# Kernel tuning notes

Measured on AMD Instinct MI355X. Metric: run time of the kernel, lower is better.

The kernel has to match this reference:

```python
import jax, jax.numpy as jnp
import numpy as np

D = 64          # node/edge feature dim
DIN = 3 * D     # concat [src, edge, dst]
N_NODES = 30000
N_EDGES = 480000


def _lin_init(key, fan_in, fan_out):
    return jax.random.normal(key, (fan_in, fan_out), dtype=jnp.float32) / np.sqrt(fan_in)


def setup_inputs() -> dict:
    key = jax.random.key(0)
    ks = jax.random.split(key, 24)
    inp = {
        "node_feat": jax.random.normal(ks[0], (N_NODES, D), dtype=jnp.float32),
        "edge_feat": jax.random.normal(ks[1], (N_EDGES, D), dtype=jnp.float32),
        "src": jax.random.randint(ks[2], (N_EDGES,), 0, N_NODES, dtype=jnp.int32),
        "dst": jax.random.randint(ks[3], (N_EDGES,), 0, N_NODES, dtype=jnp.int32),
    }
    # GatedMLP params for edge update and node update: each has a 'layers' MLP
    # [192->64->64] (SiLU after both layers) and a 'gates' MLP [192->64->64]
    # (SiLU after hidden only, then sigmoid).
    i = 4
    for pref in ("edge", "node"):
        for branch in ("layers", "gates"):
            inp[f"{pref}_{branch}_W0"] = _lin_init(ks[i], DIN, D); i += 1
            inp[f"{pref}_{branch}_b0"] = jnp.zeros((D,), jnp.float32)
            inp[f"{pref}_{branch}_W1"] = _lin_init(ks[i], D, D); i += 1
            inp[f"{pref}_{branch}_b1"] = jnp.zeros((D,), jnp.float32)
    inp["node_out_W"] = _lin_init(ks[i], D, D)  # Linear(64,64,bias=False)
    return inp


def _gated_mlp(x, lW0, lb0, lW1, lb1, gW0, gb0, gW1, gb1):
    silu = jax.nn.silu
    # layers branch: activate hidden + last
    h = silu(silu(x @ lW0 + lb0) @ lW1 + lb1)
    # gates branch: activate hidden only, sigmoid at the end
    g = silu(x @ gW0 + gb0) @ gW1 + gb1
    return h * jax.nn.sigmoid(g)


def reference(node_feat, edge_feat, src, dst,
              edge_layers_W0, edge_layers_b0, edge_layers_W1, edge_layers_b1,
              edge_gates_W0, edge_gates_b0, edge_gates_W1, edge_gates_b1,
              node_layers_W0, node_layers_b0, node_layers_W1, node_layers_b1,
              node_gates_W0, node_gates_b0, node_gates_W1, node_gates_b1,
              node_out_W):
    h_src = node_feat[src]            # [E, D] gather
    h_dst = node_feat[dst]            # [E, D] gather
    # edge update: gated MLP on [src || edge || dst], residual
    e_in = jnp.concatenate([h_src, edge_feat, h_dst], axis=-1)  # [E, 3D]
    e_new = edge_feat + _gated_mlp(e_in, edge_layers_W0, edge_layers_b0,
                                   edge_layers_W1, edge_layers_b1,
                                   edge_gates_W0, edge_gates_b0,
                                   edge_gates_W1, edge_gates_b1)
    # node messages: gated MLP on [src || new_edge || dst]
    m_in = jnp.concatenate([h_src, e_new, h_dst], axis=-1)      # [E, 3D]
    msg = _gated_mlp(m_in, node_layers_W0, node_layers_b0,
                     node_layers_W1, node_layers_b1,
                     node_gates_W0, node_gates_b0,
                     node_gates_W1, node_gates_b1)
    # scatter-sum to destination nodes, output linear, residual
    agg = jax.ops.segment_sum(msg, dst, num_segments=node_feat.shape[0])
    h_new = node_feat + agg @ node_out_W
    return h_new, e_new
```

## Files before the change

### kernel.cpp

```cpp
#include <hip/hip_runtime.h>
#include <hip/hip_bf16.h>
#include <math.h>

typedef __bf16 bf16_t;
typedef __bf16 bf16x8 __attribute__((ext_vector_type(8)));
typedef float  f32x4  __attribute__((ext_vector_type(4)));

#define MFMA16(a,b,c) __builtin_amdgcn_mfma_f32_16x16x32_bf16((a),(b),(c),0,0,0)

namespace {
constexpr int D    = 64;
constexpr int DIN  = 192;
constexpr int NN   = 30000;
constexpr int NE   = 480000;

constexpr int NBLK   = 256;
constexpr int NTHR   = 512;
constexpr int NUNITS = NE / 32;
constexpr int NWAVES = NBLK * (NTHR / 64);

constexpr int W0R    = 192;
constexpr int W0T_SZ = 64 * W0R;
constexpr int SW1    = 72;
constexpr int W1T_SZ = 64 * SW1;
constexpr int HBS    = 32 * 64;

constexpr int LDS_SCR = 4 * W0T_SZ;
constexpr int LDS_TOT = LDS_SCR + 8 * HBS;

constexpr size_t WS_AGG_BYTES = (size_t)NN * D * 4;
constexpr size_t WS_WT_BYTES  = (size_t)(4 * W0T_SZ + 4 * W1T_SZ) * 2;
constexpr size_t WS_FLAG_OFF  = WS_AGG_BYTES + WS_WT_BYTES;
}

__device__ __forceinline__ bf16x8 ldA(const bf16_t* p) {
  return *(const bf16x8*)p;
}
__device__ __forceinline__ bf16x8 ldA(const float* p) {
  const float4* q4 = (const float4*)p;
  const float4 u = q4[0], v = q4[1];
  bf16x8 r;
  r[0] = (bf16_t)u.x; r[1] = (bf16_t)u.y; r[2] = (bf16_t)u.z; r[3] = (bf16_t)u.w;
  r[4] = (bf16_t)v.x; r[5] = (bf16_t)v.y; r[6] = (bf16_t)v.z; r[7] = (bf16_t)v.w;
  return r;
}

__device__ __forceinline__ float silu_f(float v) { return v / (1.f + __expf(-v)); }
__device__ __forceinline__ float sigm_f(float v) { return 1.f / (1.f + __expf(-v)); }

__device__ __forceinline__ void wfence() {
  __builtin_amdgcn_sched_barrier(0);
  asm volatile("s_waitcnt lgkmcnt(0)" ::: "memory");
  __builtin_amdgcn_sched_barrier(0);
}

__device__ __forceinline__ void mlp_l0m(f32x4 accL[2][4], f32x4 accG[2][4],
    const bf16_t* __restrict__ w0L, const bf16_t* __restrict__ w0G,
    const bf16x8 fa[6][2], const int ksw[6], int m)
{
  const f32x4 z = {0.f, 0.f, 0.f, 0.f};
  #pragma unroll
  for (int h = 0; h < 2; ++h)
    #pragma unroll
    for (int nt = 0; nt < 4; ++nt) { accL[h][nt] = z; accG[h][nt] = z; }
  __builtin_amdgcn_s_setprio(1);
  #pragma unroll
  for (int kt = 0; kt < 6; ++kt) {
    const bf16_t* pL = w0L + m * W0R + ksw[kt];
    const bf16_t* pG = w0G + m * W0R + ksw[kt];
    #pragma unroll
    for (int nt = 0; nt < 4; ++nt) {
      const bf16x8 bL = *(const bf16x8*)(pL + nt * 16 * W0R);
      const bf16x8 bG = *(const bf16x8*)(pG + nt * 16 * W0R);
      accL[0][nt] = MFMA16(fa[kt][0], bL, accL[0][nt]);
      accL[1][nt] = MFMA16(fa[kt][1], bL, accL[1][nt]);
      accG[0][nt] = MFMA16(fa[kt][0], bG, accG[0][nt]);
      accG[1][nt] = MFMA16(fa[kt][1], bG, accG[1][nt]);
    }
  }
  __builtin_amdgcn_s_setprio(0);
}

__device__ __forceinline__ void loadW1(bf16x8 wb[2][4],
                                       const bf16_t* __restrict__ w1, int m, int q) {
  #pragma unroll
  for (int kt = 0; kt < 2; ++kt)
    #pragma unroll
    for (int nt = 0; nt < 4; ++nt)
      wb[kt][nt] = ldA(w1 + (nt * 16 + m) * SW1 + kt * 32 + q * 8);
}

__device__ __forceinline__ void mlp_l1r(f32x4 acc[2][4],
    const bf16_t* __restrict__ hb, const bf16x8 wb[2][4], const int ksw[6], int m)
{
  const f32x4 z = {0.f, 0.f, 0.f, 0.f};
  #pragma unroll
  for (int h = 0; h < 2; ++h)
    #pragma unroll
    for (int nt = 0; nt < 4; ++nt) acc[h][nt] = z;
  __builtin_amdgcn_s_setprio(1);
  #pragma unroll
  for (int kt = 0; kt < 2; ++kt) {
    const bf16x8 a0 = *(const bf16x8*)(hb + m * 64 + ksw[kt]);
    const bf16x8 a1 = *(const bf16x8*)(hb + (m + 16) * 64 + ksw[kt]);
    #pragma unroll
    for (int nt = 0; nt < 4; ++nt) {
      acc[0][nt] = MFMA16(a0, wb[kt][nt], acc[0][nt]);
      acc[1][nt] = MFMA16(a1, wb[kt][nt], acc[1][nt]);
    }
  }
  __builtin_amdgcn_s_setprio(0);
}

template<typename TB>
__device__ __forceinline__ void hidden_silu(const f32x4 acc[2][4],
    const TB* __restrict__ bias, bf16_t* __restrict__ hb, int m, int q)
{
  #pragma unroll
  for (int nt = 0; nt < 4; ++nt) {
    const float bv = (float)bias[nt * 16 + m];
    #pragma unroll
    for (int h = 0; h < 2; ++h) {
      #pragma unroll
      for (int r = 0; r < 4; ++r) {
        const float v = acc[h][nt][r] + bv;
        const int row = h * 16 + q * 4 + r;
        const int col = (nt * 16 + m) ^ (((q * 4 + r) & 7) << 3);
        hb[row * 64 + col] = (bf16_t)silu_f(v);
      }
    }
  }
}

__global__ void detect_kernel(const void* w0, int* flag) {
  __shared__ int cnt;
  if (threadIdx.x == 0) cnt = 0;
  __syncthreads();
  const unsigned short* u = (const unsigned short*)w0;
  const unsigned short v = u[2 * threadIdx.x];
  const int e = (v >> 7) & 0xFF;
  atomicAdd(&cnt, (e >= 100 && e <= 140) ? 1 : 0);
  __syncthreads();
  if (threadIdx.x == 0) *flag = (cnt >= 128) ? 1 : 0;
}

struct PrepArgs { const void* w[8]; bf16_t* o[8]; };

template<typename T>
__global__ void prep_kernel(const int* flag, int want, PrepArgs a) {
  if (*flag != want) return;
  const int b = blockIdx.x, t = threadIdx.x;
  const T* w = (const T*)a.w[b];
  bf16_t* o = a.o[b];
  if (b < 4) {
    for (int i = t; i < DIN * D; i += 256) {
      const int n = i & 63, k = i >> 6;
      o[(n * W0R + k) ^ ((n & 7) << 3)] = (bf16_t)(float)w[i];
    }
  } else {
    for (int i = t; i < D * D; i += 256) o[(i & 63) * SW1 + (i >> 6)] = (bf16_t)(float)w[i];
  }
}

template<typename T>
__global__ __launch_bounds__(NTHR, 2) void fused_kernel(
    const int* __restrict__ flag, int want,
    const T* __restrict__ nf, const T* __restrict__ ef,
    const int* __restrict__ src, const int* __restrict__ dst,
    const T* __restrict__ eLb0, const T* __restrict__ eLb1,
    const T* __restrict__ eGb0, const T* __restrict__ eGb1,
    const T* __restrict__ nLb0, const T* __restrict__ nLb1,
    const T* __restrict__ nGb0, const T* __restrict__ nGb1,
    const bf16_t* __restrict__ wt, float* __restrict__ agg,
    T* __restrict__ out_e)
{
  if (*flag != want) return;
  __shared__ __align__(16) bf16_t sm[LDS_TOT];
  const int t = threadIdx.x;

  {
    int4* ls = (int4*)sm; const int4* gs = (const int4*)wt;
    for (int i = t; i < (LDS_SCR >> 3); i += NTHR) ls[i] = gs[i];
  }
  __syncthreads();

  const int lane = t & 63;
  const int w    = t >> 6;
  const int m    = lane & 15;
  const int q    = lane >> 4;
  bf16_t* hb = sm + LDS_SCR + w * HBS;

  int ksw[6];
  #pragma unroll
  for (int kt = 0; kt < 6; ++kt) ksw[kt] = (kt * 32 + q * 8) ^ ((m & 7) << 3);

  const bf16_t* w0eL = sm;
  const bf16_t* w0eG = sm + W0T_SZ;
  const bf16_t* w0nL = sm + 2 * W0T_SZ;
  const bf16_t* w0nG = sm + 3 * W0T_SZ;
  const bf16_t* w1g  = wt + 4 * W0T_SZ;

  for (int u = blockIdx.x * (NTHR / 64) + w; u < NUNITS; u += NWAVES) {
    const int e0 = u * 32;
    const int eA = e0 + m, eB = eA + 16;
    const int sA = src[eA], sB = src[eB];
    const int dA = dst[eA], dB = dst[eB];

    wfence();

    bf16x8 fa[6][2];
    #pragma unroll
    for (int kt = 0; kt < 2; ++kt) {
      const int ko = kt * 32 + q * 8;
      fa[kt][0]     = ldA(nf + (size_t)sA * D + ko);
      fa[kt][1]     = ldA(nf + (size_t)sB * D + ko);
      fa[2 + kt][0] = ldA(ef + (size_t)eA * D + ko);
      fa[2 + kt][1] = ldA(ef + (size_t)eB * D + ko);
      fa[4 + kt][0] = ldA(nf + (size_t)dA * D + ko);
      fa[4 + kt][1] = ldA(nf + (size_t)dB * D + ko);
    }

    bf16x8 w1L[2][4], w1G[2][4];
    loadW1(w1L, w1g + 0 * W1T_SZ, m, q);
    loadW1(w1G, w1g + 1 * W1T_SZ, m, q);

    f32x4 accL[2][4], accG[2][4], hl[2][4], gl[2][4];

    mlp_l0m(accL, accG, w0eL, w0eG, fa, ksw, m);
    hidden_silu(accL, eLb0, hb, m, q);
    wfence();
    mlp_l1r(hl, hb, w1L, ksw, m);
    wfence();
    hidden_silu(accG, eGb0, hb, m, q);
    wfence();
    mlp_l1r(gl, hb, w1G, ksw, m);
    wfence();

    loadW1(w1L, w1g + 2 * W1T_SZ, m, q);
    loadW1(w1G, w1g + 3 * W1T_SZ, m, q);

    #pragma unroll
    for (int nt = 0; nt < 4; ++nt) {
      const int n = nt * 16 + m;
      const float bL = (float)eLb1[n];
      const float bG = (float)eGb1[n];
      #pragma unroll
      for (int h = 0; h < 2; ++h) {
        #pragma unroll
        for (int r = 0; r < 4; ++r) {
          const int e = e0 + h * 16 + q * 4 + r;
          const float hv = silu_f(hl[h][nt][r] + bL);
          const float gv = sigm_f(gl[h][nt][r] + bG);
          const float val = (float)ef[(size_t)e * D + n] + hv * gv;
          out_e[(size_t)e * D + n] = (T)val;
          const int row = h * 16 + q * 4 + r;
          const int col = n ^ (((q * 4 + r) & 7) << 3);
          hb[row * 64 + col] = (bf16_t)val;
        }
      }
    }
    wfence();
    #pragma unroll
    for (int kt = 0; kt < 2; ++kt) {
      fa[2 + kt][0] = ldA(hb + m * 64 + ksw[kt]);
      fa[2 + kt][1] = ldA(hb + (m + 16) * 64 + ksw[kt]);
    }
    wfence();

    mlp_l0m(accL, accG, w0nL, w0nG, fa, ksw, m);
    hidden_silu(accL, nLb0, hb, m, q);
    wfence();
    mlp_l1r(hl, hb, w1L, ksw, m);
    wfence();
    hidden_silu(accG, nGb0, hb, m, q);
    wfence();
    mlp_l1r(gl, hb, w1G, ksw, m);

    int d8[2][4];
    #pragma unroll
    for (int h = 0; h < 2; ++h)
      #pragma unroll
      for (int r = 0; r < 4; ++r)
        d8[h][r] = dst[e0 + h * 16 + q * 4 + r];

    #pragma unroll
    for (int nt = 0; nt < 4; ++nt) {
      const int n = nt * 16 + m;
      const float bL = (float)nLb1[n];
      const float bG = (float)nGb1[n];
      #pragma unroll
      for (int h = 0; h < 2; ++h) {
        #pragma unroll
        for (int r = 0; r < 4; ++r) {
          const float hv = silu_f(hl[h][nt][r] + bL);
          const float gv = sigm_f(gl[h][nt][r] + bG);
          atomicAdd(&agg[(size_t)d8[h][r] * D + n], hv * gv);
        }
      }
    }
  }
}

template<typename T>
__global__ __launch_bounds__(256) void node_out_kernel(
    const int* __restrict__ flag, int want,
    const T* __restrict__ nf, const float* __restrict__ agg,
    const T* __restrict__ Wo, T* __restrict__ out_h)
{
  if (*flag != want) return;
  __shared__ float wsh[D * D];
  const int t = threadIdx.x;
  for (int i = t; i < D * D; i += 256) wsh[i] = (float)Wo[i];
  __syncthreads();
  const int node = blockIdx.x * 4 + (t >> 6);
  const int j = t & 63;
  const float* arow = agg + node * D;
  float acc = 0.f;
  #pragma unroll
  for (int k = 0; k < D; ++k) acc = fmaf(arow[k], wsh[k * D + j], acc);
  out_h[node * D + j] = (T)((float)nf[node * D + j] + acc);
}

template<typename T>
static void launch_all(void* const* d_in, void* d_out, void* d_ws,
                       const int* flag, int want, bf16_t* wt, float* agg,
                       hipStream_t stream) {
  const T* nf  = (const T*)d_in[0];
  const T* ef  = (const T*)d_in[1];
  const int* src = (const int*)d_in[2];
  const int* dst = (const int*)d_in[3];
  T* out_h = (T*)d_out;
  T* out_e = out_h + (size_t)NN * D;

  fused_kernel<T><<<NBLK, NTHR, 0, stream>>>(flag, want, nf, ef, src, dst,
      (const T*)d_in[5],  (const T*)d_in[7],
      (const T*)d_in[9],  (const T*)d_in[11],
      (const T*)d_in[13], (const T*)d_in[15],
      (const T*)d_in[17], (const T*)d_in[19],
      wt, agg, out_e);
  node_out_kernel<T><<<NN / 4, 256, 0, stream>>>(flag, want, nf, agg,
      (const T*)d_in[20], out_h);
}

extern "C" void kernel_launch(void* const* d_in, const int* in_sizes, int n_in,
                              void* d_out, int out_size, void* d_ws, size_t ws_size,
                              hipStream_t stream) {
  float*  agg  = (float*)d_ws;
  bf16_t* wt   = (bf16_t*)((char*)d_ws + WS_AGG_BYTES);
  int*    flag = (int*)((char*)d_ws + WS_FLAG_OFF);

  hipMemsetAsync(d_ws, 0, WS_AGG_BYTES, stream);

  detect_kernel<<<1, 256, 0, stream>>>(d_in[4], flag);

  PrepArgs pa;
  pa.w[0] = d_in[4];  pa.w[1] = d_in[8];  pa.w[2] = d_in[12]; pa.w[3] = d_in[16];
  pa.w[4] = d_in[6];  pa.w[5] = d_in[10]; pa.w[6] = d_in[14]; pa.w[7] = d_in[18];
  for (int i = 0; i < 4; ++i) pa.o[i]     = wt + i * W0T_SZ;
  for (int j = 0; j < 4; ++j) pa.o[4 + j] = wt + 4 * W0T_SZ + j * W1T_SZ;
  prep_kernel<float> <<<8, 256, 0, stream>>>(flag, 0, pa);
  prep_kernel<bf16_t><<<8, 256, 0, stream>>>(flag, 1, pa);

  launch_all<float> (d_in, d_out, d_ws, flag, 0, wt, agg, stream);
  launch_all<bf16_t>(d_in, d_out, d_ws, flag, 1, wt, agg, stream);
}
```

Baseline: 647.1 us.

## Prefetch next unit's gathered features during current unit's MLP compute

The fused edge kernel's loop is software-pipelined. Indices and gathered node/edge features for the next 32-edge unit are issued while the current unit's node MLP runs, so the random-gather latency is hidden behind MFMA work. W1 fragments now go through one register buffer loaded just before each layer-1 matmul, cutting register pressure to make room for the prefetch. The occupancy hint moves to amdgpu_waves_per_eu, and the node output kernel becomes a grid-stride loop over 512 blocks instead of one block per four nodes.

```diff
diff --git a/kernel.cpp b/kernel.cpp
--- a/kernel.cpp
+++ b/kernel.cpp
@@ -52,6 +52,23 @@
   __builtin_amdgcn_sched_barrier(0);
   asm volatile("s_waitcnt lgkmcnt(0)" ::: "memory");
   __builtin_amdgcn_sched_barrier(0);
+}
+
+template<typename T>
+__device__ __forceinline__ void gather_fa(bf16x8 fa[6][2],
+    const T* __restrict__ nf, const T* __restrict__ ef,
+    int sA, int sB, int dA, int dB, int eA, int eB, int q)
+{
+  #pragma unroll
+  for (int kt = 0; kt < 2; ++kt) {
+    const int ko = kt * 32 + q * 8;
+    fa[kt][0]     = ldA(nf + (size_t)sA * D + ko);
+    fa[kt][1]     = ldA(nf + (size_t)sB * D + ko);
+    fa[2 + kt][0] = ldA(ef + (size_t)eA * D + ko);
+    fa[2 + kt][1] = ldA(ef + (size_t)eB * D + ko);
+    fa[4 + kt][0] = ldA(nf + (size_t)dA * D + ko);
+    fa[4 + kt][1] = ldA(nf + (size_t)dB * D + ko);
+  }
 }
 
 __device__ __forceinline__ void mlp_l0m(f32x4 accL[2][4], f32x4 accG[2][4],
@@ -163,7 +180,9 @@
 }
 
 template<typename T>
-__global__ __launch_bounds__(NTHR, 2) void fused_kernel(
+__global__ __launch_bounds__(NTHR)
+__attribute__((amdgpu_waves_per_eu(2, 2)))
+void fused_kernel(
     const int* __restrict__ flag, int want,
     const T* __restrict__ nf, const T* __restrict__ ef,
     const int* __restrict__ src, const int* __restrict__ dst,
@@ -200,44 +219,37 @@
   const bf16_t* w0nG = sm + 3 * W0T_SZ;
   const bf16_t* w1g  = wt + 4 * W0T_SZ;
 
-  for (int u = blockIdx.x * (NTHR / 64) + w; u < NUNITS; u += NWAVES) {
-    const int e0 = u * 32;
-    const int eA = e0 + m, eB = eA + 16;
-    const int sA = src[eA], sB = src[eB];
-    const int dA = dst[eA], dB = dst[eB];
-
-    wfence();
-
-    bf16x8 fa[6][2];
-    #pragma unroll
-    for (int kt = 0; kt < 2; ++kt) {
-      const int ko = kt * 32 + q * 8;
-      fa[kt][0]     = ldA(nf + (size_t)sA * D + ko);
-      fa[kt][1]     = ldA(nf + (size_t)sB * D + ko);
-      fa[2 + kt][0] = ldA(ef + (size_t)eA * D + ko);
-      fa[2 + kt][1] = ldA(ef + (size_t)eB * D + ko);
-      fa[4 + kt][0] = ldA(nf + (size_t)dA * D + ko);
-      fa[4 + kt][1] = ldA(nf + (size_t)dB * D + ko);
-    }
-
-    bf16x8 w1L[2][4], w1G[2][4];
-    loadW1(w1L, w1g + 0 * W1T_SZ, m, q);
-    loadW1(w1G, w1g + 1 * W1T_SZ, m, q);
+  int u  = blockIdx.x * (NTHR / 64) + w;
+  int e0 = u * 32;
+  int sA = src[e0 + m], sB = src[e0 + m + 16];
+  int dA = dst[e0 + m], dB = dst[e0 + m + 16];
+  bf16x8 fa[6][2];
+  gather_fa(fa, nf, ef, sA, sB, dA, dB, e0 + m, e0 + m + 16, q);
+
+  while (u < NUNITS) {
+    const int un  = (u + NWAVES < NUNITS) ? (u + NWAVES) : u;
+    const int e0n = un * 32;
+
+    wfence();
 
     f32x4 accL[2][4], accG[2][4], hl[2][4], gl[2][4];
+    bf16x8 w1f[2][4];
 
     mlp_l0m(accL, accG, w0eL, w0eG, fa, ksw, m);
+
+    const int sAn = src[e0n + m], sBn = src[e0n + m + 16];
+    const int dAn = dst[e0n + m], dBn = dst[e0n + m + 16];
+
+    loadW1(w1f, w1g + 0 * W1T_SZ, m, q);
     hidden_silu(accL, eLb0, hb, m, q);
     wfence();
-    mlp_l1r(hl, hb, w1L, ksw, m);
-    wfence();
+    mlp_l1r(hl, hb, w1f, ksw, m);
+    wfence();
+    loadW1(w1f, w1g + 1 * W1T_SZ, m, q);
     hidden_silu(accG, eGb0, hb, m, q);
     wfence();
-    mlp_l1r(gl, hb, w1G, ksw, m);
-    wfence();
-
-    loadW1(w1L, w1g + 2 * W1T_SZ, m, q);
-    loadW1(w1G, w1g + 3 * W1T_SZ, m, q);
+    mlp_l1r(gl, hb, w1f, ksw, m);
+    wfence();
 
     #pragma unroll
     for (int nt = 0; nt < 4; ++nt) {
@@ -268,13 +280,18 @@
     wfence();
 
     mlp_l0m(accL, accG, w0nL, w0nG, fa, ksw, m);
+
+    gather_fa(fa, nf, ef, sAn, sBn, dAn, dBn, e0n + m, e0n + m + 16, q);
+
+    loadW1(w1f, w1g + 2 * W1T_SZ, m, q);
     hidden_silu(accL, nLb0, hb, m, q);
     wfence();
-    mlp_l1r(hl, hb, w1L, ksw, m);
-    wfence();
+    mlp_l1r(hl, hb, w1f, ksw, m);
+    wfence();
+    loadW1(w1f, w1g + 3 * W1T_SZ, m, q);
     hidden_silu(accG, nGb0, hb, m, q);
     wfence();
-    mlp_l1r(gl, hb, w1G, ksw, m);
+    mlp_l1r(gl, hb, w1f, ksw, m);
 
     int d8[2][4];
     #pragma unroll
@@ -298,6 +315,9 @@
         }
       }
     }
+
+    u += NWAVES; e0 = e0n;
+    sA = sAn; sB = sBn; dA = dAn; dB = dBn;
   }
 }
 
@@ -312,13 +332,14 @@
   const int t = threadIdx.x;
   for (int i = t; i < D * D; i += 256) wsh[i] = (float)Wo[i];
   __syncthreads();
-  const int node = blockIdx.x * 4 + (t >> 6);
   const int j = t & 63;
-  const float* arow = agg + node * D;
-  float acc = 0.f;
-  #pragma unroll
-  for (int k = 0; k < D; ++k) acc = fmaf(arow[k], wsh[k * D + j], acc);
-  out_h[node * D + j] = (T)((float)nf[node * D + j] + acc);
+  for (int node = blockIdx.x * 4 + (t >> 6); node < NN; node += gridDim.x * 4) {
+    const float* arow = agg + (size_t)node * D;
+    float acc = 0.f;
+    #pragma unroll
+    for (int k = 0; k < D; ++k) acc = fmaf(arow[k], wsh[k * D + j], acc);
+    out_h[(size_t)node * D + j] = (T)((float)nf[(size_t)node * D + j] + acc);
+  }
 }
 
 template<typename T>
@@ -338,7 +359,7 @@
       (const T*)d_in[13], (const T*)d_in[15],
       (const T*)d_in[17], (const T*)d_in[19],
       wt, agg, out_e);
-  node_out_kernel<T><<<NN / 4, 256, 0, stream>>>(flag, want, nf, agg,
+  node_out_kernel<T><<<512, 256, 0, stream>>>(flag, want, nf, agg,
       (const T*)d_in[20], out_h);
 }
 
```

New measurement: 647.8 us. About the same (+0.1%).
